# Performance work log

Measured on AMD Instinct MI355X. Metric: run time of the kernel, lower is better.

Reference implementation:

```python
import jax, jax.numpy as jnp
import numpy as np

NUM_EXPERTS = 8
HIDDEN = 1024
INTER = 2048
RANK = 8
LORA_ALPHA = 16
SCALING = LORA_ALPHA / RANK  # 2.0


def setup_inputs() -> dict:
    key = jax.random.key(0)
    ks = jax.random.split(key, 7)
    return {
        "hidden_states": jax.random.normal(ks[0], (NUM_EXPERTS * 1024, HIDDEN), jnp.float32),
        "gate_up_proj": jax.random.normal(ks[1], (NUM_EXPERTS, HIDDEN, 2 * INTER), jnp.float32) * 0.02,
        "down_proj": jax.random.normal(ks[2], (NUM_EXPERTS, INTER, HIDDEN), jnp.float32) * 0.02,
        "lora_A_gu": jax.random.normal(ks[3], (RANK, HIDDEN), jnp.float32) * 0.02,
        "lora_B_gu": jax.random.normal(ks[4], (2 * INTER, RANK), jnp.float32) * 0.02,
        "lora_A_dn": jax.random.normal(ks[5], (RANK, INTER), jnp.float32) * 0.02,
        "lora_B_dn": jax.random.normal(ks[6], (1024, RANK), jnp.float32) * 0.02,
    }


def reference(hidden_states, gate_up_proj, down_proj, lora_A_gu, lora_B_gu, lora_A_dn, lora_B_dn):
    E, H, F2 = gate_up_proj.shape
    x = hidden_states.reshape(E, -1, H)  # [E, T, H]
    # per-expert GEMM + shared LoRA adapter (dropout inactive at eval)
    gate_up = jnp.einsum('eth,ehf->etf', x, gate_up_proj)
    gate_up = gate_up + ((x @ lora_A_gu.T) @ lora_B_gu.T) * SCALING  # [E, T, 2I]
    gate, up = jnp.split(gate_up, 2, axis=-1)
    hidden = up * jax.nn.silu(gate)  # SwiGLU, [E, T, I]
    out = jnp.einsum('eti,eih->eth', hidden, down_proj)
    out = out + ((hidden @ lora_A_dn.T) @ lora_B_dn.T) * SCALING
    return out.reshape(-1, H)
```

## Files before the change

kernel.cpp:

```cpp
#include <hip/hip_runtime.h>
#include <math.h>


#define NE 8
#define TT 1024
#define HH 1024
#define II 2048
#define FF2 4096
#define RR 8
#define NROW (NE * TT)
#define SCAL 2.0f

typedef __bf16 bf16x8 __attribute__((ext_vector_type(8)));
typedef float f32x4 __attribute__((ext_vector_type(4)));

#define GLOAD16(g, l)                                                        \
  __builtin_amdgcn_global_load_lds((const __attribute__((address_space(1))) void*)(g), \
                                   (__attribute__((address_space(3))) void*)(l), 16, 0, 0)
#define BARRIER __builtin_amdgcn_s_barrier()
#define SB0 __builtin_amdgcn_sched_barrier(0)
#define WAITV8 asm volatile("s_waitcnt vmcnt(8)" ::: "memory")
#define WAITV0 asm volatile("s_waitcnt vmcnt(0)" ::: "memory")
#define WAITL0 asm volatile("s_waitcnt lgkmcnt(0)" ::: "memory")

__device__ __forceinline__ unsigned short f2bf(float f) {
  unsigned int u = __float_as_uint(f);
  u += 0x7fffu + ((u >> 16) & 1u);
  return (unsigned short)(u >> 16);
}
__device__ __forceinline__ float dot4(float4 a, float4 b) {
  return a.x * b.x + a.y * b.y + a.z * b.z + a.w * b.w;
}

__global__ __launch_bounds__(256) void convx_kernel(const float* __restrict__ x,
                                                    unsigned short* __restrict__ xb) {
  const int i = blockIdx.x * 256 + threadIdx.x;
  const float4 a = *(const float4*)(x + (size_t)i * 8);
  const float4 b = *(const float4*)(x + (size_t)i * 8 + 4);
  union { unsigned short u[8]; uint4 v; } pk;
  pk.u[0] = f2bf(a.x); pk.u[1] = f2bf(a.y); pk.u[2] = f2bf(a.z); pk.u[3] = f2bf(a.w);
  pk.u[4] = f2bf(b.x); pk.u[5] = f2bf(b.y); pk.u[6] = f2bf(b.z); pk.u[7] = f2bf(b.w);
  *(uint4*)(xb + (size_t)i * 8) = pk.v;
}

__global__ __launch_bounds__(256) void transconv_gu_kernel(const float* __restrict__ W,
                                                           unsigned short* __restrict__ WT) {
  __shared__ float ts[64][65];
  const int bid = blockIdx.x;
  const int nt = bid & 63, kt = (bid >> 6) & 15, e = bid >> 10;
  const float* Win = W + (size_t)e * HH * FF2 + (size_t)(kt * 64) * FF2 + nt * 64;
  const int tid = threadIdx.x;
#pragma unroll
  for (int l = 0; l < 4; ++l) {
    const int idx = tid + l * 256, r = idx >> 4, c4 = idx & 15;
    const float4 v = *(const float4*)(Win + (size_t)r * FF2 + c4 * 4);
    ts[r][c4 * 4 + 0] = v.x; ts[r][c4 * 4 + 1] = v.y;
    ts[r][c4 * 4 + 2] = v.z; ts[r][c4 * 4 + 3] = v.w;
  }
  __syncthreads();
  unsigned short* We = WT + (size_t)e * FF2 * HH;
#pragma unroll
  for (int l = 0; l < 2; ++l) {
    const int idx = tid + l * 256, j = idx >> 3, q = idx & 7;
    int orow;
    if (nt < 32) orow = (nt * 4 + (j >> 4)) * 32 + (j & 15);
    else         orow = ((nt - 32) * 4 + (j >> 4)) * 32 + 16 + (j & 15);
    union { unsigned short u[8]; uint4 v; } pk;
#pragma unroll
    for (int kk = 0; kk < 8; ++kk) pk.u[kk] = f2bf(ts[q * 8 + kk][j]);
    *(uint4*)(We + (size_t)orow * HH + kt * 64 + q * 8) = pk.v;
  }
}

__global__ __launch_bounds__(256) void transconv_dn_kernel(const float* __restrict__ W,
                                                           unsigned short* __restrict__ WT) {
  __shared__ float ts[64][65];
  const int bid = blockIdx.x;
  const int nt = bid & 15, kt = (bid >> 4) & 31, e = bid >> 9;
  const float* Win = W + (size_t)e * II * HH + (size_t)(kt * 64) * HH + nt * 64;
  const int tid = threadIdx.x;
#pragma unroll
  for (int l = 0; l < 4; ++l) {
    const int idx = tid + l * 256, r = idx >> 4, c4 = idx & 15;
    const float4 v = *(const float4*)(Win + (size_t)r * HH + c4 * 4);
    ts[r][c4 * 4 + 0] = v.x; ts[r][c4 * 4 + 1] = v.y;
    ts[r][c4 * 4 + 2] = v.z; ts[r][c4 * 4 + 3] = v.w;
  }
  __syncthreads();
  unsigned short* Wout = WT + (size_t)e * HH * II + (size_t)(nt * 64) * II + kt * 64;
#pragma unroll
  for (int l = 0; l < 2; ++l) {
    const int idx = tid + l * 256, j = idx >> 3, q = idx & 7;
    union { unsigned short u[8]; uint4 v; } pk;
#pragma unroll
    for (int kk = 0; kk < 8; ++kk) pk.u[kk] = f2bf(ts[q * 8 + kk][j]);
    *(uint4*)(Wout + (size_t)j * II + q * 8) = pk.v;
  }
}

template <int K>
__global__ __launch_bounds__(256) void rowdot_kernel(const float* __restrict__ x,
                                                     const float* __restrict__ A,
                                                     float* __restrict__ xa) {
  const int w = threadIdx.x >> 6, lane = threadIdx.x & 63;
  const int t = blockIdx.x * 4 + w;
  const float* xrow = x + (size_t)t * K;
  float acc[RR];
#pragma unroll
  for (int r = 0; r < RR; ++r) acc[r] = 0.f;
#pragma unroll
  for (int c = 0; c < K / 256; ++c) {
    const float4 xv = *(const float4*)(xrow + c * 256 + lane * 4);
#pragma unroll
    for (int r = 0; r < RR; ++r) {
      const float4 av = *(const float4*)(A + (size_t)r * K + c * 256 + lane * 4);
      acc[r] += dot4(xv, av);
    }
  }
#pragma unroll
  for (int r = 0; r < RR; ++r) {
    float v = acc[r];
#pragma unroll
    for (int off = 32; off > 0; off >>= 1) v += __shfl_down(v, off, 64);
    if (lane == 0) xa[(size_t)t * RR + r] = v;
  }
}

__global__ __launch_bounds__(256) void rowdot_bf16_kernel(const unsigned short* __restrict__ h,
                                                          const float* __restrict__ A,
                                                          float* __restrict__ ha) {
  const int w = threadIdx.x >> 6, lane = threadIdx.x & 63;
  const int t = blockIdx.x * 4 + w;
  const unsigned short* hrow = h + (size_t)t * II;
  float acc[RR];
#pragma unroll
  for (int r = 0; r < RR; ++r) acc[r] = 0.f;
#pragma unroll
  for (int c = 0; c < II / 512; ++c) {
    const uint4 v = *(const uint4*)(hrow + c * 512 + lane * 8);
    float xv[8];
    xv[0] = __uint_as_float(v.x << 16); xv[1] = __uint_as_float(v.x & 0xffff0000u);
    xv[2] = __uint_as_float(v.y << 16); xv[3] = __uint_as_float(v.y & 0xffff0000u);
    xv[4] = __uint_as_float(v.z << 16); xv[5] = __uint_as_float(v.z & 0xffff0000u);
    xv[6] = __uint_as_float(v.w << 16); xv[7] = __uint_as_float(v.w & 0xffff0000u);
#pragma unroll
    for (int r = 0; r < RR; ++r) {
      const float4 a0 = *(const float4*)(A + (size_t)r * II + c * 512 + lane * 8);
      const float4 a1 = *(const float4*)(A + (size_t)r * II + c * 512 + lane * 8 + 4);
      acc[r] += xv[0] * a0.x + xv[1] * a0.y + xv[2] * a0.z + xv[3] * a0.w +
                xv[4] * a1.x + xv[5] * a1.y + xv[6] * a1.z + xv[7] * a1.w;
    }
  }
#pragma unroll
  for (int r = 0; r < RR; ++r) {
    float v = acc[r];
#pragma unroll
    for (int off = 32; off > 0; off >>= 1) v += __shfl_down(v, off, 64);
    if (lane == 0) ha[(size_t)t * RR + r] = v;
  }
}

__global__ __launch_bounds__(256) void gemm1_8p_kernel(
    const unsigned short* __restrict__ xb, const unsigned short* __restrict__ WguT,
    const float* __restrict__ xa, const float* __restrict__ Bgu,
    unsigned short* __restrict__ hidden) {
  __shared__ unsigned short sm[2][16384];

  const int bid = blockIdx.x;
  const int e = bid & 7;
  const int s = bid >> 3;
  const int g = s >> 6, wq = s & 63;
  const int tt = wq >> 3, it = (g << 3) | (wq & 7);
  const int t0 = e * TT + tt * 128;
  const unsigned short* Ag = xb + (size_t)t0 * HH;
  const unsigned short* Bg = WguT + (size_t)e * FF2 * HH + (size_t)(it * 128) * HH;

  const int tid = threadIdx.x;
  const int w = tid >> 6, lane = tid & 63;
  const int wr = w >> 1, wc = w & 1;
  const int lrow = lane & 15, lkg = lane >> 4;

  auto stageA = [&](int buf, int kt, int h) {
#pragma unroll
    for (int l = 0; l < 2; ++l) {
      const int i = tid + l * 256;
      const int r = i >> 3, sl = i & 7;
      const int row = h * 64 + r;
      GLOAD16((const char*)(Ag + (size_t)row * HH + kt * 64 + ((sl ^ (row & 7)) << 3)),
              (char*)&sm[buf][0] + row * 128 + sl * 16);
    }
  };
  auto stageB = [&](int buf, int kt, int h) {
#pragma unroll
    for (int l = 0; l < 2; ++l) {
      const int i = tid + l * 256;
      const int r = i >> 3, sl = i & 7;
      const int row = h * 64 + r;
      GLOAD16((const char*)(Bg + (size_t)row * HH + kt * 64 + ((sl ^ (row & 7)) << 3)),
              (char*)&sm[buf][0] + 16384 + row * 128 + sl * 16);
    }
  };
  auto ldA = [&](int p, int mIdx, int s2) -> bf16x8 {
    const int row = wr * 64 + mIdx * 16 + lrow;
    const int sl = (s2 * 4 + lkg) ^ (row & 7);
    return *(const bf16x8*)((const char*)&sm[p][0] + row * 128 + sl * 16);
  };
  auto ldB = [&](int p, int nj, int s2) -> bf16x8 {
    const int row = wc * 64 + nj * 16 + lrow;
    const int sl = (s2 * 4 + lkg) ^ (row & 7);
    return *(const bf16x8*)((const char*)&sm[p][0] + 16384 + row * 128 + sl * 16);
  };

  f32x4 acc[4][4];
#pragma unroll
  for (int i = 0; i < 4; ++i)
#pragma unroll
    for (int j = 0; j < 4; ++j) acc[i][j] = (f32x4)(0.f);

  stageA(0, 0, 0); stageA(0, 0, 1); stageB(0, 0, 0); stageB(0, 0, 1);

  const int NT = HH / 64;
  for (int t = 0; t < NT; ++t) {
    const int p = t & 1, q = p ^ 1;
    if (t + 1 < NT) {
      stageA(q, t + 1, 0); stageA(q, t + 1, 1);
      stageB(q, t + 1, 0); stageB(q, t + 1, 1);
      WAITV8;
    } else {
      WAITV0;
    }
    SB0; BARRIER;
    bf16x8 af[4][2], bfr[4][2];
#pragma unroll
    for (int mi = 0; mi < 4; ++mi) { af[mi][0] = ldA(p, mi, 0); af[mi][1] = ldA(p, mi, 1); }
#pragma unroll
    for (int nj = 0; nj < 4; ++nj) { bfr[nj][0] = ldB(p, nj, 0); bfr[nj][1] = ldB(p, nj, 1); }
    WAITL0; SB0;
    __builtin_amdgcn_s_setprio(1);
#pragma unroll
    for (int mi = 0; mi < 4; ++mi)
#pragma unroll
      for (int nj = 0; nj < 4; ++nj)
#pragma unroll
        for (int s2 = 0; s2 < 2; ++s2)
          acc[mi][nj] = __builtin_amdgcn_mfma_f32_16x16x32_bf16(af[mi][s2], bfr[nj][s2], acc[mi][nj], 0, 0, 0);
    __builtin_amdgcn_s_setprio(0); SB0; BARRIER;
  }

  const float4* xa4 = (const float4*)xa;
  const float4* B4 = (const float4*)Bgu;
#pragma unroll
  for (int f = 0; f < 2; ++f) {
    const int gc = it * 64 + (wc * 2 + f) * 16 + lrow;
    const float4 bg0 = B4[gc * 2], bg1 = B4[gc * 2 + 1];
    const float4 bu0 = B4[(II + gc) * 2], bu1 = B4[(II + gc) * 2 + 1];
#pragma unroll
    for (int m = 0; m < 4; ++m) {
      const int tb = t0 + wr * 64 + m * 16 + lkg * 4;
#pragma unroll
      for (int j = 0; j < 4; ++j) {
        const int trow = tb + j;
        const float4 xr0 = xa4[trow * 2], xr1 = xa4[trow * 2 + 1];
        const float gv = acc[m][f * 2 + 0][j] + SCAL * (dot4(xr0, bg0) + dot4(xr1, bg1));
        const float uv = acc[m][f * 2 + 1][j] + SCAL * (dot4(xr0, bu0) + dot4(xr1, bu1));
        const float sg = gv / (1.f + __expf(-gv));
        hidden[(size_t)trow * II + gc] = f2bf(uv * sg);
      }
    }
  }
}

__global__ __launch_bounds__(256) void gemm2_8p_kernel(
    const unsigned short* __restrict__ hid, const unsigned short* __restrict__ WdnT,
    const float* __restrict__ ha, const float* __restrict__ Bdn,
    float* __restrict__ out) {
  __shared__ unsigned short sm[2][16384];

  const int bid = blockIdx.x;
  const int e = bid & 7;
  const int s = bid >> 3;
  const int g = s >> 4, wq = s & 15;
  const int tt = (g >> 1) * 4 + (wq >> 2);
  const int ht = (g & 1) * 4 + (wq & 3);
  const int t0 = e * TT + tt * 128;
  const int h0 = ht * 128;
  const unsigned short* Ag = hid + (size_t)t0 * II;
  const unsigned short* Bg = WdnT + (size_t)e * HH * II + (size_t)h0 * II;

  const int tid = threadIdx.x;
  const int w = tid >> 6, lane = tid & 63;
  const int wr = w >> 1, wc = w & 1;
  const int lrow = lane & 15, lkg = lane >> 4;

  auto stageA = [&](int buf, int kt, int h) {
#pragma unroll
    for (int l = 0; l < 2; ++l) {
      const int i = tid + l * 256;
      const int r = i >> 3, sl = i & 7;
      const int row = h * 64 + r;
      GLOAD16((const char*)(Ag + (size_t)row * II + kt * 64 + ((sl ^ (row & 7)) << 3)),
              (char*)&sm[buf][0] + row * 128 + sl * 16);
    }
  };
  auto stageB = [&](int buf, int kt, int h) {
#pragma unroll
    for (int l = 0; l < 2; ++l) {
      const int i = tid + l * 256;
      const int r = i >> 3, sl = i & 7;
      const int row = h * 64 + r;
      GLOAD16((const char*)(Bg + (size_t)row * II + kt * 64 + ((sl ^ (row & 7)) << 3)),
              (char*)&sm[buf][0] + 16384 + row * 128 + sl * 16);
    }
  };
  auto ldA = [&](int p, int mIdx, int s2) -> bf16x8 {
    const int row = wr * 64 + mIdx * 16 + lrow;
    const int sl = (s2 * 4 + lkg) ^ (row & 7);
    return *(const bf16x8*)((const char*)&sm[p][0] + row * 128 + sl * 16);
  };
  auto ldB = [&](int p, int nj, int s2) -> bf16x8 {
    const int row = wc * 64 + nj * 16 + lrow;
    const int sl = (s2 * 4 + lkg) ^ (row & 7);
    return *(const bf16x8*)((const char*)&sm[p][0] + 16384 + row * 128 + sl * 16);
  };

  f32x4 acc[4][4];
#pragma unroll
  for (int i = 0; i < 4; ++i)
#pragma unroll
    for (int j = 0; j < 4; ++j) acc[i][j] = (f32x4)(0.f);

  stageA(0, 0, 0); stageA(0, 0, 1); stageB(0, 0, 0); stageB(0, 0, 1);

  const int NT = II / 64;
  for (int t = 0; t < NT; ++t) {
    const int p = t & 1, q = p ^ 1;
    if (t + 1 < NT) {
      stageA(q, t + 1, 0); stageA(q, t + 1, 1);
      stageB(q, t + 1, 0); stageB(q, t + 1, 1);
      WAITV8;
    } else {
      WAITV0;
    }
    SB0; BARRIER;
    bf16x8 af[4][2], bfr[4][2];
#pragma unroll
    for (int mi = 0; mi < 4; ++mi) { af[mi][0] = ldA(p, mi, 0); af[mi][1] = ldA(p, mi, 1); }
#pragma unroll
    for (int nj = 0; nj < 4; ++nj) { bfr[nj][0] = ldB(p, nj, 0); bfr[nj][1] = ldB(p, nj, 1); }
    WAITL0; SB0;
    __builtin_amdgcn_s_setprio(1);
#pragma unroll
    for (int mi = 0; mi < 4; ++mi)
#pragma unroll
      for (int nj = 0; nj < 4; ++nj)
#pragma unroll
        for (int s2 = 0; s2 < 2; ++s2)
          acc[mi][nj] = __builtin_amdgcn_mfma_f32_16x16x32_bf16(af[mi][s2], bfr[nj][s2], acc[mi][nj], 0, 0, 0);
    __builtin_amdgcn_s_setprio(0); SB0; BARRIER;
  }

  const float4* ha4 = (const float4*)ha;
  const float4* B4 = (const float4*)Bdn;
#pragma unroll
  for (int nj = 0; nj < 4; ++nj) {
    const int col = h0 + wc * 64 + nj * 16 + lrow;
    const float4 b0 = B4[col * 2], b1 = B4[col * 2 + 1];
#pragma unroll
    for (int m = 0; m < 4; ++m) {
      const int tb = t0 + wr * 64 + m * 16 + lkg * 4;
#pragma unroll
      for (int j = 0; j < 4; ++j) {
        const int trow = tb + j;
        const float4 hr0 = ha4[trow * 2], hr1 = ha4[trow * 2 + 1];
        out[(size_t)trow * HH + col] = acc[m][nj][j] + SCAL * (dot4(hr0, b0) + dot4(hr1, b1));
      }
    }
  }
}

__global__ __launch_bounds__(256) void gemm1_conv_kernel(const float* __restrict__ x,
                                                         const float* __restrict__ Wgu,
                                                         const float* __restrict__ xa,
                                                         const float* __restrict__ Bgu,
                                                         unsigned short* __restrict__ hidden) {
  __shared__ unsigned short As[128][40];
  __shared__ unsigned short Bs[128][40];
  const int bid = blockIdx.x;
  const int e = bid >> 8, rem = bid & 255, tt = rem >> 5, it = rem & 31;
  const int t0 = e * TT + tt * 128, i0 = it * 64;
  const float* Wg = Wgu + (size_t)e * HH * FF2;
  const int tid = threadIdx.x, w = tid >> 6, lane = tid & 63;
  const int wr = w >> 1, wc = w & 1, lrow = lane & 15, lk = (lane >> 4) * 8;
  f32x4 acc[4][4];
#pragma unroll
  for (int i = 0; i < 4; ++i)
#pragma unroll
    for (int j = 0; j < 4; ++j) acc[i][j] = (f32x4)(0.f);
  for (int k0 = 0; k0 < HH; k0 += 32) {
#pragma unroll
    for (int l = 0; l < 4; ++l) {
      const int idx = tid + l * 256, row = idx >> 3, kq = idx & 7;
      const float4 v = *(const float4*)(x + (size_t)(t0 + row) * HH + k0 + kq * 4);
      ushort4 p; p.x = f2bf(v.x); p.y = f2bf(v.y); p.z = f2bf(v.z); p.w = f2bf(v.w);
      *(ushort4*)&As[row][kq * 4] = p;
    }
#pragma unroll
    for (int l = 0; l < 2; ++l) {
      const int idx = tid + l * 256, col = idx & 127, kq8 = idx >> 7;
      const int gcol = i0 + (col & 63) + ((col >> 6) * II);
      union { unsigned short u[8]; uint4 v; } pk;
#pragma unroll
      for (int kk = 0; kk < 8; ++kk) pk.u[kk] = f2bf(Wg[(size_t)(k0 + kq8 * 8 + kk) * FF2 + gcol]);
      *(uint4*)&Bs[col][kq8 * 8] = pk.v;
    }
    __syncthreads();
    bf16x8 af[4], bfr[4];
#pragma unroll
    for (int mi = 0; mi < 4; ++mi) af[mi] = *(const bf16x8*)&As[wr * 64 + mi * 16 + lrow][lk];
#pragma unroll
    for (int nj = 0; nj < 4; ++nj) {
      const int c = (nj < 2) ? (wc * 32 + nj * 16) : (64 + wc * 32 + (nj - 2) * 16);
      bfr[nj] = *(const bf16x8*)&Bs[c + lrow][lk];
    }
#pragma unroll
    for (int mi = 0; mi < 4; ++mi)
#pragma unroll
      for (int nj = 0; nj < 4; ++nj)
        acc[mi][nj] = __builtin_amdgcn_mfma_f32_16x16x32_bf16(af[mi], bfr[nj], acc[mi][nj], 0, 0, 0);
    __syncthreads();
  }
  const float4* xa4 = (const float4*)xa;
  const float4* B4 = (const float4*)Bgu;
#pragma unroll
  for (int nj = 0; nj < 2; ++nj) {
    const int coln = i0 + wc * 32 + nj * 16 + lrow;
    const float4 bg0 = B4[coln * 2], bg1 = B4[coln * 2 + 1];
    const float4 bu0 = B4[(II + coln) * 2], bu1 = B4[(II + coln) * 2 + 1];
#pragma unroll
    for (int mi = 0; mi < 4; ++mi) {
      const int tb = t0 + wr * 64 + mi * 16 + (lane >> 4) * 4;
#pragma unroll
      for (int j = 0; j < 4; ++j) {
        const int t = tb + j;
        const float4 xr0 = xa4[t * 2], xr1 = xa4[t * 2 + 1];
        const float g = acc[mi][nj][j] + SCAL * (dot4(xr0, bg0) + dot4(xr1, bg1));
        const float u = acc[mi][nj + 2][j] + SCAL * (dot4(xr0, bu0) + dot4(xr1, bu1));
        const float s = g / (1.f + __expf(-g));
        hidden[(size_t)t * II + coln] = f2bf(u * s);
      }
    }
  }
}

__global__ __launch_bounds__(256) void gemm2_conv_kernel(const unsigned short* __restrict__ hid,
                                                         const float* __restrict__ Wdn,
                                                         const float* __restrict__ ha,
                                                         const float* __restrict__ Bdn,
                                                         float* __restrict__ out) {
  __shared__ unsigned short As[128][40];
  __shared__ unsigned short Bs[128][40];
  const int bid = blockIdx.x;
  const int e = bid >> 6, rem = bid & 63, tt = rem >> 3, ht = rem & 7;
  const int t0 = e * TT + tt * 128, h0 = ht * 128;
  const float* Wd = Wdn + (size_t)e * II * HH;
  const int tid = threadIdx.x, w = tid >> 6, lane = tid & 63;
  const int wr = w >> 1, wc = w & 1, lrow = lane & 15, lk = (lane >> 4) * 8;
  f32x4 acc[4][4];
#pragma unroll
  for (int i = 0; i < 4; ++i)
#pragma unroll
    for (int j = 0; j < 4; ++j) acc[i][j] = (f32x4)(0.f);
  for (int k0 = 0; k0 < II; k0 += 32) {
#pragma unroll
    for (int l = 0; l < 2; ++l) {
      const int idx = tid + l * 256, row = idx >> 2, kq8 = idx & 3;
      *(uint4*)&As[row][kq8 * 8] = *(const uint4*)(hid + (size_t)(t0 + row) * II + k0 + kq8 * 8);
    }
#pragma unroll
    for (int l = 0; l < 2; ++l) {
      const int idx = tid + l * 256, col = idx & 127, kq8 = idx >> 7;
      union { unsigned short u[8]; uint4 v; } pk;
#pragma unroll
      for (int kk = 0; kk < 8; ++kk) pk.u[kk] = f2bf(Wd[(size_t)(k0 + kq8 * 8 + kk) * HH + h0 + col]);
      *(uint4*)&Bs[col][kq8 * 8] = pk.v;
    }
    __syncthreads();
    bf16x8 af[4], bfr[4];
#pragma unroll
    for (int mi = 0; mi < 4; ++mi) af[mi] = *(const bf16x8*)&As[wr * 64 + mi * 16 + lrow][lk];
#pragma unroll
    for (int nj = 0; nj < 4; ++nj) bfr[nj] = *(const bf16x8*)&Bs[wc * 64 + nj * 16 + lrow][lk];
#pragma unroll
    for (int mi = 0; mi < 4; ++mi)
#pragma unroll
      for (int nj = 0; nj < 4; ++nj)
        acc[mi][nj] = __builtin_amdgcn_mfma_f32_16x16x32_bf16(af[mi], bfr[nj], acc[mi][nj], 0, 0, 0);
    __syncthreads();
  }
  const float4* ha4 = (const float4*)ha;
  const float4* B4 = (const float4*)Bdn;
#pragma unroll
  for (int nj = 0; nj < 4; ++nj) {
    const int coln = h0 + wc * 64 + nj * 16 + lrow;
    const float4 b0 = B4[coln * 2], b1 = B4[coln * 2 + 1];
#pragma unroll
    for (int mi = 0; mi < 4; ++mi) {
      const int tb = t0 + wr * 64 + mi * 16 + (lane >> 4) * 4;
#pragma unroll
      for (int j = 0; j < 4; ++j) {
        const int t = tb + j;
        const float4 hr0 = ha4[t * 2], hr1 = ha4[t * 2 + 1];
        out[(size_t)t * HH + coln] = acc[mi][nj][j] + SCAL * (dot4(hr0, b0) + dot4(hr1, b1));
      }
    }
  }
}

extern "C" void kernel_launch(void* const* d_in, const int* in_sizes, int n_in,
                              void* d_out, int out_size, void* d_ws, size_t ws_size,
                              hipStream_t stream) {
  const float* x   = (const float*)d_in[0];
  const float* Wgu = (const float*)d_in[1];
  const float* Wdn = (const float*)d_in[2];
  const float* Agu = (const float*)d_in[3];
  const float* Bgu = (const float*)d_in[4];
  const float* Adn = (const float*)d_in[5];
  const float* Bdn = (const float*)d_in[6];
  float* out = (float*)d_out;

  char* ws = (char*)d_ws;
  unsigned short* hidden = (unsigned short*)ws;
  const size_t OFF_XB  = (size_t)NROW * II * 2;
  const size_t OFF_WGU = OFF_XB + (size_t)NROW * HH * 2;
  const size_t OFF_WDN = OFF_WGU + (size_t)NE * FF2 * HH * 2;
  const size_t OFF_XA  = OFF_WDN + (size_t)NE * HH * II * 2;
  const size_t OFF_HA  = OFF_XA + (size_t)NROW * RR * 4;
  const size_t NEED    = OFF_HA + (size_t)NROW * RR * 4;

  if (ws_size >= NEED) {
    unsigned short* xb   = (unsigned short*)(ws + OFF_XB);
    unsigned short* WguT = (unsigned short*)(ws + OFF_WGU);
    unsigned short* WdnT = (unsigned short*)(ws + OFF_WDN);
    float* xa = (float*)(ws + OFF_XA);
    float* ha = (float*)(ws + OFF_HA);

    convx_kernel<<<(NROW * HH) / (256 * 8), 256, 0, stream>>>(x, xb);
    transconv_gu_kernel<<<NE * 16 * 64, 256, 0, stream>>>(Wgu, WguT);
    transconv_dn_kernel<<<NE * 32 * 16, 256, 0, stream>>>(Wdn, WdnT);
    rowdot_kernel<HH><<<NROW / 4, 256, 0, stream>>>(x, Agu, xa);
    gemm1_8p_kernel<<<NE * 8 * 32, 256, 0, stream>>>(xb, WguT, xa, Bgu, hidden);
    rowdot_bf16_kernel<<<NROW / 4, 256, 0, stream>>>(hidden, Adn, ha);
    gemm2_8p_kernel<<<NE * 8 * 8, 256, 0, stream>>>(hidden, WdnT, ha, Bdn, out);
  } else {
    float* xa = (float*)(ws + OFF_XB);
    float* ha = xa + (size_t)NROW * RR;
    rowdot_kernel<HH><<<NROW / 4, 256, 0, stream>>>(x, Agu, xa);
    gemm1_conv_kernel<<<NE * 8 * 32, 256, 0, stream>>>(x, Wgu, xa, Bgu, hidden);
    rowdot_bf16_kernel<<<NROW / 4, 256, 0, stream>>>(hidden, Adn, ha);
    gemm2_conv_kernel<<<NE * 8 * 8, 256, 0, stream>>>(hidden, Wdn, ha, Bdn, out);
  }
}
```

Baseline: 357.6 us.

## Replace double-buffered LDS pipeline with single buffer and higher occupancy in GEMMs

Both expert GEMM kernels drop the double-buffered LDS prefetch, which used hand-placed waitcnt, sched barriers and setprio. They now use a single 32KB buffer that is loaded and then synchronised with __syncthreads each k-step. Launch bounds request 3 blocks per CU, so the intent is to hide memory latency through more resident workgroups instead of in-block software pipelining. The risk is that global-to-LDS loads no longer overlap MFMA work within a block, and two full barriers per iteration are added.

```diff
diff --git a/kernel.cpp b/kernel.cpp
--- a/kernel.cpp
+++ b/kernel.cpp
@@ -17,11 +17,6 @@
 #define GLOAD16(g, l)                                                        \
   __builtin_amdgcn_global_load_lds((const __attribute__((address_space(1))) void*)(g), \
                                    (__attribute__((address_space(3))) void*)(l), 16, 0, 0)
-#define BARRIER __builtin_amdgcn_s_barrier()
-#define SB0 __builtin_amdgcn_sched_barrier(0)
-#define WAITV8 asm volatile("s_waitcnt vmcnt(8)" ::: "memory")
-#define WAITV0 asm volatile("s_waitcnt vmcnt(0)" ::: "memory")
-#define WAITL0 asm volatile("s_waitcnt lgkmcnt(0)" ::: "memory")
 
 __device__ __forceinline__ unsigned short f2bf(float f) {
   unsigned int u = __float_as_uint(f);
@@ -160,11 +155,11 @@
   }
 }
 
-__global__ __launch_bounds__(256) void gemm1_8p_kernel(
+__global__ __launch_bounds__(256, 3) void gemm1_8p_kernel(
     const unsigned short* __restrict__ xb, const unsigned short* __restrict__ WguT,
     const float* __restrict__ xa, const float* __restrict__ Bgu,
     unsigned short* __restrict__ hidden) {
-  __shared__ unsigned short sm[2][16384];
+  __shared__ unsigned short sm[16384];
 
   const int bid = blockIdx.x;
   const int e = bid & 7;
@@ -180,35 +175,27 @@
   const int wr = w >> 1, wc = w & 1;
   const int lrow = lane & 15, lkg = lane >> 4;
 
-  auto stageA = [&](int buf, int kt, int h) {
-#pragma unroll
-    for (int l = 0; l < 2; ++l) {
+  auto stage = [&](int kt) {
+#pragma unroll
+    for (int l = 0; l < 4; ++l) {
       const int i = tid + l * 256;
       const int r = i >> 3, sl = i & 7;
-      const int row = h * 64 + r;
-      GLOAD16((const char*)(Ag + (size_t)row * HH + kt * 64 + ((sl ^ (row & 7)) << 3)),
-              (char*)&sm[buf][0] + row * 128 + sl * 16);
+      const int off = kt * 64 + ((sl ^ (r & 7)) << 3);
+      GLOAD16((const char*)(Ag + (size_t)r * HH + off),
+              (char*)&sm[0] + r * 128 + sl * 16);
+      GLOAD16((const char*)(Bg + (size_t)r * HH + off),
+              (char*)&sm[0] + 16384 + r * 128 + sl * 16);
     }
   };
-  auto stageB = [&](int buf, int kt, int h) {
-#pragma unroll
-    for (int l = 0; l < 2; ++l) {
-      const int i = tid + l * 256;
-      const int r = i >> 3, sl = i & 7;
-      const int row = h * 64 + r;
-      GLOAD16((const char*)(Bg + (size_t)row * HH + kt * 64 + ((sl ^ (row & 7)) << 3)),
-              (char*)&sm[buf][0] + 16384 + row * 128 + sl * 16);
-    }
-  };
-  auto ldA = [&](int p, int mIdx, int s2) -> bf16x8 {
+  auto ldA = [&](int mIdx, int s2) -> bf16x8 {
     const int row = wr * 64 + mIdx * 16 + lrow;
     const int sl = (s2 * 4 + lkg) ^ (row & 7);
-    return *(const bf16x8*)((const char*)&sm[p][0] + row * 128 + sl * 16);
+    return *(const bf16x8*)((const char*)&sm[0] + row * 128 + sl * 16);
   };
-  auto ldB = [&](int p, int nj, int s2) -> bf16x8 {
+  auto ldB = [&](int nj, int s2) -> bf16x8 {
     const int row = wc * 64 + nj * 16 + lrow;
     const int sl = (s2 * 4 + lkg) ^ (row & 7);
-    return *(const bf16x8*)((const char*)&sm[p][0] + 16384 + row * 128 + sl * 16);
+    return *(const bf16x8*)((const char*)&sm[0] + 16384 + row * 128 + sl * 16);
   };
 
   f32x4 acc[4][4];
@@ -216,27 +203,16 @@
   for (int i = 0; i < 4; ++i)
 #pragma unroll
     for (int j = 0; j < 4; ++j) acc[i][j] = (f32x4)(0.f);
-
-  stageA(0, 0, 0); stageA(0, 0, 1); stageB(0, 0, 0); stageB(0, 0, 1);
 
   const int NT = HH / 64;
   for (int t = 0; t < NT; ++t) {
-    const int p = t & 1, q = p ^ 1;
-    if (t + 1 < NT) {
-      stageA(q, t + 1, 0); stageA(q, t + 1, 1);
-      stageB(q, t + 1, 0); stageB(q, t + 1, 1);
-      WAITV8;
-    } else {
-      WAITV0;
-    }
-    SB0; BARRIER;
+    stage(t);
+    __syncthreads();
     bf16x8 af[4][2], bfr[4][2];
 #pragma unroll
-    for (int mi = 0; mi < 4; ++mi) { af[mi][0] = ldA(p, mi, 0); af[mi][1] = ldA(p, mi, 1); }
-#pragma unroll
-    for (int nj = 0; nj < 4; ++nj) { bfr[nj][0] = ldB(p, nj, 0); bfr[nj][1] = ldB(p, nj, 1); }
-    WAITL0; SB0;
-    __builtin_amdgcn_s_setprio(1);
+    for (int mi = 0; mi < 4; ++mi) { af[mi][0] = ldA(mi, 0); af[mi][1] = ldA(mi, 1); }
+#pragma unroll
+    for (int nj = 0; nj < 4; ++nj) { bfr[nj][0] = ldB(nj, 0); bfr[nj][1] = ldB(nj, 1); }
 #pragma unroll
     for (int mi = 0; mi < 4; ++mi)
 #pragma unroll
@@ -244,7 +220,7 @@
 #pragma unroll
         for (int s2 = 0; s2 < 2; ++s2)
           acc[mi][nj] = __builtin_amdgcn_mfma_f32_16x16x32_bf16(af[mi][s2], bfr[nj][s2], acc[mi][nj], 0, 0, 0);
-    __builtin_amdgcn_s_setprio(0); SB0; BARRIER;
+    __syncthreads();
   }
 
   const float4* xa4 = (const float4*)xa;
@@ -270,11 +246,11 @@
   }
 }
 
-__global__ __launch_bounds__(256) void gemm2_8p_kernel(
+__global__ __launch_bounds__(256, 3) void gemm2_8p_kernel(
     const unsigned short* __restrict__ hid, const unsigned short* __restrict__ WdnT,
     const float* __restrict__ ha, const float* __restrict__ Bdn,
     float* __restrict__ out) {
-  __shared__ unsigned short sm[2][16384];
+  __shared__ unsigned short sm[16384];
 
   const int bid = blockIdx.x;
   const int e = bid & 7;
@@ -292,35 +268,27 @@
   const int wr = w >> 1, wc = w & 1;
   const int lrow = lane & 15, lkg = lane >> 4;
 
-  auto stageA = [&](int buf, int kt, int h) {
-#pragma unroll
-    for (int l = 0; l < 2; ++l) {
+  auto stage = [&](int kt) {
+#pragma unroll
+    for (int l = 0; l < 4; ++l) {
       const int i = tid + l * 256;
       const int r = i >> 3, sl = i & 7;
-      const int row = h * 64 + r;
-      GLOAD16((const char*)(Ag + (size_t)row * II + kt * 64 + ((sl ^ (row & 7)) << 3)),
-              (char*)&sm[buf][0] + row * 128 + sl * 16);
+      const int off = kt * 64 + ((sl ^ (r & 7)) << 3);
+      GLOAD16((const char*)(Ag + (size_t)r * II + off),
+              (char*)&sm[0] + r * 128 + sl * 16);
+      GLOAD16((const char*)(Bg + (size_t)r * II + off),
+              (char*)&sm[0] + 16384 + r * 128 + sl * 16);
     }
   };
-  auto stageB = [&](int buf, int kt, int h) {
-#pragma unroll
-    for (int l = 0; l < 2; ++l) {
-      const int i = tid + l * 256;
-      const int r = i >> 3, sl = i & 7;
-      const int row = h * 64 + r;
-      GLOAD16((const char*)(Bg + (size_t)row * II + kt * 64 + ((sl ^ (row & 7)) << 3)),
-              (char*)&sm[buf][0] + 16384 + row * 128 + sl * 16);
-    }
-  };
-  auto ldA = [&](int p, int mIdx, int s2) -> bf16x8 {
+  auto ldA = [&](int mIdx, int s2) -> bf16x8 {
     const int row = wr * 64 + mIdx * 16 + lrow;
     const int sl = (s2 * 4 + lkg) ^ (row & 7);
-    return *(const bf16x8*)((const char*)&sm[p][0] + row * 128 + sl * 16);
+    return *(const bf16x8*)((const char*)&sm[0] + row * 128 + sl * 16);
   };
-  auto ldB = [&](int p, int nj, int s2) -> bf16x8 {
+  auto ldB = [&](int nj, int s2) -> bf16x8 {
     const int row = wc * 64 + nj * 16 + lrow;
     const int sl = (s2 * 4 + lkg) ^ (row & 7);
-    return *(const bf16x8*)((const char*)&sm[p][0] + 16384 + row * 128 + sl * 16);
+    return *(const bf16x8*)((const char*)&sm[0] + 16384 + row * 128 + sl * 16);
   };
 
   f32x4 acc[4][4];
@@ -328,27 +296,16 @@
   for (int i = 0; i < 4; ++i)
 #pragma unroll
     for (int j = 0; j < 4; ++j) acc[i][j] = (f32x4)(0.f);
-
-  stageA(0, 0, 0); stageA(0, 0, 1); stageB(0, 0, 0); stageB(0, 0, 1);
 
   const int NT = II / 64;
   for (int t = 0; t < NT; ++t) {
-    const int p = t & 1, q = p ^ 1;
-    if (t + 1 < NT) {
-      stageA(q, t + 1, 0); stageA(q, t + 1, 1);
-      stageB(q, t + 1, 0); stageB(q, t + 1, 1);
-      WAITV8;
-    } else {
-      WAITV0;
-    }
-    SB0; BARRIER;
+    stage(t);
+    __syncthreads();
     bf16x8 af[4][2], bfr[4][2];
 #pragma unroll
-    for (int mi = 0; mi < 4; ++mi) { af[mi][0] = ldA(p, mi, 0); af[mi][1] = ldA(p, mi, 1); }
-#pragma unroll
-    for (int nj = 0; nj < 4; ++nj) { bfr[nj][0] = ldB(p, nj, 0); bfr[nj][1] = ldB(p, nj, 1); }
-    WAITL0; SB0;
-    __builtin_amdgcn_s_setprio(1);
+    for (int mi = 0; mi < 4; ++mi) { af[mi][0] = ldA(mi, 0); af[mi][1] = ldA(mi, 1); }
+#pragma unroll
+    for (int nj = 0; nj < 4; ++nj) { bfr[nj][0] = ldB(nj, 0); bfr[nj][1] = ldB(nj, 1); }
 #pragma unroll
     for (int mi = 0; mi < 4; ++mi)
 #pragma unroll
@@ -356,7 +313,7 @@
 #pragma unroll
         for (int s2 = 0; s2 < 2; ++s2)
           acc[mi][nj] = __builtin_amdgcn_mfma_f32_16x16x32_bf16(af[mi][s2], bfr[nj][s2], acc[mi][nj], 0, 0, 0);
-    __builtin_amdgcn_s_setprio(0); SB0; BARRIER;
+    __syncthreads();
   }
 
   const float4* ha4 = (const float4*)ha;
```

Result: slower. 526.0 us (+47.1%).
